# Kernel optimization log

Hardware: AMD Instinct MI355X
Metric: run time of the kernel (lower is better)

The kernel has to match this reference:

```python
import jax, jax.numpy as jnp
import numpy as np

N_NODES = 100000
N_EDGES = 1250000
D_FEAT = 64


def setup_inputs() -> dict:
    key = jax.random.key(0)
    kx, ke = jax.random.split(key)
    x = jax.random.normal(kx, (N_NODES, D_FEAT), dtype=jnp.float32)
    edge_index = jax.random.randint(ke, (2, N_EDGES), 0, N_NODES, dtype=jnp.int64)
    return {"x": x, "edge_index": edge_index}


def reference(x, edge_index):
    # propagate: scatter_nested gathers x[idxj] grouped by destination idxi
    # (a ragged per-node neighbor set); the module's sum_nested reduces each
    # group. Expressed densely and jit-ably as gather + segment-sum.
    idxi = edge_index[0, :]  # destination nodes
    idxj = edge_index[1, :]  # source nodes
    messages = x[idxj]  # [E, D] edge-level gather (memory-bound)
    out = jax.ops.segment_sum(messages, idxi, num_segments=N_NODES)  # [N, D]
    return out
```

## Files before the change

kernel.cpp:

```cpp
#include <hip/hip_runtime.h>

#define N_NODES 100000
#define N_EDGES 1250000
#define D_FEAT  64

#define NPB     256
#define NBINS   ((N_NODES + NPB - 1) / NPB)
#define BCAP    4096
#define EPB     4096
#define K1B     ((N_EDGES + EPB - 1) / EPB)
#define OVF_CAP 32768

#define CAP     48


__global__ __launch_bounds__(512) void k1_bin_kernel(
        const int* __restrict__ idxi, const int* __restrict__ idxj,
        int* __restrict__ gcursor, int* __restrict__ ovfcnt,
        int* __restrict__ ovf, int* __restrict__ binbuf) {
    __shared__ int hist[512];
    __shared__ int runstart[512];
    __shared__ int gbase[NBINS];
    __shared__ int cur[NBINS];
    __shared__ int staged[EPB];
    __shared__ unsigned short sbin[EPB];
    int t = threadIdx.x;
    hist[t] = 0;
    __syncthreads();

    long long base = (long long)blockIdx.x * EPB;
    int d[8], s[8], bn[8];
#pragma unroll
    for (int j = 0; j < 8; ++j) {
        long long e = base + t + j * 512;
        if (e < N_EDGES) {
            d[j] = idxi[e];
            s[j] = idxj[e];
            bn[j] = d[j] >> 8;
            atomicAdd(&hist[bn[j]], 1);
        } else {
            bn[j] = -1;
        }
    }
    __syncthreads();

    runstart[t] = hist[t];
    __syncthreads();
    for (int off = 1; off < 512; off <<= 1) {
        int add = (t >= off) ? runstart[t - off] : 0;
        __syncthreads();
        runstart[t] += add;
        __syncthreads();
    }
    int excl = runstart[t] - hist[t];
    __syncthreads();
    runstart[t] = excl;
    if (t < NBINS) {
        gbase[t] = hist[t] ? atomicAdd(&gcursor[t], hist[t]) : 0;
        cur[t] = 0;
    }
    __syncthreads();

#pragma unroll
    for (int j = 0; j < 8; ++j) {
        if (bn[j] >= 0) {
            int lofs = atomicAdd(&cur[bn[j]], 1);
            int idx = runstart[bn[j]] + lofs;
            staged[idx] = ((d[j] & 255) << 17) | s[j];
            sbin[idx] = (unsigned short)bn[j];
        }
    }
    __syncthreads();

    long long rem = (long long)N_EDGES - base;
    int n = (rem < EPB) ? (int)rem : EPB;
    for (int i = t; i < n; i += 512) {
        int b = sbin[i];
        int p = staged[i];
        int tgt = gbase[b] + (i - runstart[b]);
        if (tgt < BCAP) {
            binbuf[(size_t)b * BCAP + tgt] = p;
        } else {
            int op = atomicAdd(ovfcnt, 1);
            if (op < OVF_CAP) { ovf[2 * op] = b * NPB + (p >> 17); ovf[2 * op + 1] = p & 0x1FFFF; }
        }
    }
}

__global__ __launch_bounds__(1024) void k2_sort_kernel(
        const int* __restrict__ gcursor, const int* __restrict__ binbuf,
        int* __restrict__ sorted, int* __restrict__ offs, int* __restrict__ len) {
    __shared__ int cnt[NPB];
    __shared__ int excl[NPB];
    __shared__ int cur[NPB];
    __shared__ int stmp[NPB];
    int bin = blockIdx.x;
    int t = threadIdx.x;
    if (t < NPB) cnt[t] = 0;
    __syncthreads();

    int n = gcursor[bin];
    if (n > BCAP) n = BCAP;
    const int* src = binbuf + (size_t)bin * BCAP;
    int p[4];
#pragma unroll
    for (int j = 0; j < 4; ++j) {
        int i = t + j * 1024;
        p[j] = (i < n) ? src[i] : -1;
        if (p[j] >= 0) atomicAdd(&cnt[p[j] >> 17], 1);
    }
    __syncthreads();

    if (t < NPB) stmp[t] = cnt[t];
    __syncthreads();
    for (int off = 1; off < NPB; off <<= 1) {
        int v = 0;
        if (t < NPB && t >= off) v = stmp[t - off];
        __syncthreads();
        if (t < NPB) stmp[t] += v;
        __syncthreads();
    }
    if (t < NPB) {
        excl[t] = stmp[t] - cnt[t];
        cur[t] = 0;
        int node = bin * NPB + t;
        if (node < N_NODES) {
            offs[node] = bin * BCAP + excl[t];
            len[node]  = cnt[t];
        }
    }
    __syncthreads();

    int* dst = sorted + (size_t)bin * BCAP;
#pragma unroll
    for (int j = 0; j < 4; ++j) {
        if (p[j] >= 0) {
            int dl = p[j] >> 17;
            int pos = excl[dl] + atomicAdd(&cur[dl], 1);
            dst[pos] = p[j] & 0x1FFFF;
        }
    }
}

__global__ __launch_bounds__(256) void k3_gather_kernel(
        const float* __restrict__ x, const int* __restrict__ offs,
        const int* __restrict__ len, const int* __restrict__ sorted,
        float* __restrict__ out) {
    int node = blockIdx.x * 4 + (threadIdx.x >> 6);
    int lane = threadIdx.x & 63;
    if (node >= N_NODES) return;
    const int* b = sorted + offs[node];
    int l = len[node];
    int sub = lane >> 4;
    int c4  = lane & 15;

    float4 acc = make_float4(0.f, 0.f, 0.f, 0.f);
    int k = 0;
    for (; k + 8 <= l; k += 8) {
        int s0 = b[k + sub];
        int s1 = b[k + 4 + sub];
        const float4 v0 = *(const float4*)(x + (size_t)s0 * D_FEAT + c4 * 4);
        const float4 v1 = *(const float4*)(x + (size_t)s1 * D_FEAT + c4 * 4);
        acc.x += v0.x + v1.x;
        acc.y += v0.y + v1.y;
        acc.z += v0.z + v1.z;
        acc.w += v0.w + v1.w;
    }
    if (k + 4 <= l) {
        int s0 = b[k + sub];
        const float4 v0 = *(const float4*)(x + (size_t)s0 * D_FEAT + c4 * 4);
        acc.x += v0.x; acc.y += v0.y; acc.z += v0.z; acc.w += v0.w;
        k += 4;
    }
    if (k + sub < l) {
        int s0 = b[k + sub];
        const float4 v0 = *(const float4*)(x + (size_t)s0 * D_FEAT + c4 * 4);
        acc.x += v0.x; acc.y += v0.y; acc.z += v0.z; acc.w += v0.w;
    }

    acc.x += __shfl_xor(acc.x, 16, 64);
    acc.y += __shfl_xor(acc.y, 16, 64);
    acc.z += __shfl_xor(acc.z, 16, 64);
    acc.w += __shfl_xor(acc.w, 16, 64);
    acc.x += __shfl_xor(acc.x, 32, 64);
    acc.y += __shfl_xor(acc.y, 32, 64);
    acc.z += __shfl_xor(acc.z, 32, 64);
    acc.w += __shfl_xor(acc.w, 32, 64);

    if (lane < 16) {
        ((float4*)out)[(size_t)node * 16 + c4] = acc;
    }
}

__global__ __launch_bounds__(256) void ovf_fixup_kernel(
        const float* __restrict__ x, const int* __restrict__ ovfcnt,
        const int* __restrict__ ovf, float* __restrict__ out) {
    int n = *ovfcnt;
    if (n > OVF_CAP) n = OVF_CAP;
    long long total = (long long)n * 16;
    long long stride = (long long)gridDim.x * blockDim.x;
    for (long long t = blockIdx.x * blockDim.x + threadIdx.x; t < total; t += stride) {
        int e  = (int)(t >> 4);
        int fo = ((int)t & 15) << 2;
        int d = ovf[2 * e];
        int s = ovf[2 * e + 1];
        const float4 v = *(const float4*)(x + (size_t)s * D_FEAT + fo);
        float* o = out + (size_t)d * D_FEAT + fo;
        atomicAdd(o + 0, v.x);
        atomicAdd(o + 1, v.y);
        atomicAdd(o + 2, v.z);
        atomicAdd(o + 3, v.w);
    }
}


__global__ __launch_bounds__(256) void scatter_pad_kernel(
        const int* __restrict__ idxi, const int* __restrict__ idxj,
        int* __restrict__ cnt, int* __restrict__ ovfcnt,
        int* __restrict__ ovf, int* __restrict__ bucket) {
    int e = blockIdx.x * blockDim.x + threadIdx.x;
    if (e >= N_EDGES) return;
    int d = idxi[e];
    int s = idxj[e];
    int pos = atomicAdd(&cnt[d], 1);
    if (pos < CAP) {
        bucket[(size_t)d * CAP + pos] = s;
    } else {
        int op = atomicAdd(ovfcnt, 1);
        if (op < OVF_CAP) { ovf[2 * op] = d; ovf[2 * op + 1] = s; }
    }
}

__global__ __launch_bounds__(256) void gather_pad_kernel(
        const float* __restrict__ x, const int* __restrict__ cnt,
        const int* __restrict__ bucket, float* __restrict__ out) {
    int node = blockIdx.x * 4 + (threadIdx.x >> 6);
    int lane = threadIdx.x & 63;
    if (node >= N_NODES) return;
    int c = cnt[node];
    if (c > CAP) c = CAP;
    const int* b = bucket + (size_t)node * CAP;
    float acc = 0.f;
    int k = 0;
    for (; k + 4 <= c; k += 4) {
        int4 s4 = *(const int4*)(b + k);
        float a0 = x[(size_t)s4.x * D_FEAT + lane];
        float a1 = x[(size_t)s4.y * D_FEAT + lane];
        float a2 = x[(size_t)s4.z * D_FEAT + lane];
        float a3 = x[(size_t)s4.w * D_FEAT + lane];
        acc += (a0 + a1) + (a2 + a3);
    }
    for (; k < c; ++k) acc += x[(size_t)b[k] * D_FEAT + lane];
    out[(size_t)node * D_FEAT + lane] = acc;
}


__global__ __launch_bounds__(256) void zero_f4_kernel(float* __restrict__ out, int n4) {
    int i = blockIdx.x * blockDim.x + threadIdx.x;
    if (i < n4) ((float4*)out)[i] = make_float4(0.f, 0.f, 0.f, 0.f);
}

__global__ __launch_bounds__(256) void scatter_add_kernel(const float* __restrict__ x,
                                                          const int* __restrict__ idxi,
                                                          const int* __restrict__ idxj,
                                                          float* __restrict__ out) {
    int t = blockIdx.x * blockDim.x + threadIdx.x;
    int e = t >> 4;
    if (e >= N_EDGES) return;
    int fo = (t & 15) << 2;
    int dst = idxi[e];
    int src = idxj[e];
    const float4 v = *(const float4*)(x + (size_t)src * D_FEAT + fo);
    float* o = out + (size_t)dst * D_FEAT + fo;
    atomicAdd(o + 0, v.x);
    atomicAdd(o + 1, v.y);
    atomicAdd(o + 2, v.z);
    atomicAdd(o + 3, v.w);
}

extern "C" void kernel_launch(void* const* d_in, const int* in_sizes, int n_in,
                              void* d_out, int out_size, void* d_ws, size_t ws_size,
                              hipStream_t stream) {
    const float* x  = (const float*)d_in[0];
    const int*   ei = (const int*)d_in[1];
    const int*   idxi = ei;
    const int*   idxj = ei + N_EDGES;
    float* out = (float*)d_out;

    int nbe = (N_EDGES + 255) / 256;
    int gather_blocks = (N_NODES + 3) / 4;

    {
        size_t need = (512 + 16 + 2 * (size_t)OVF_CAP +
                       2 * (size_t)NBINS * BCAP + 2 * (size_t)N_NODES) * sizeof(int);
        if (ws_size >= need) {
            int* gcursor = (int*)d_ws;
            int* ovfcnt  = gcursor + 512;
            int* ovf     = ovfcnt + 16;
            int* binbuf  = ovf + 2 * OVF_CAP;
            int* sorted  = binbuf + (size_t)NBINS * BCAP;
            int* offs    = sorted + (size_t)NBINS * BCAP;
            int* len     = offs + N_NODES;

            hipMemsetAsync(gcursor, 0, (512 + 16) * sizeof(int), stream);
            k1_bin_kernel<<<K1B, 512, 0, stream>>>(idxi, idxj, gcursor, ovfcnt, ovf, binbuf);
            k2_sort_kernel<<<NBINS, 1024, 0, stream>>>(gcursor, binbuf, sorted, offs, len);
            k3_gather_kernel<<<gather_blocks, 256, 0, stream>>>(x, offs, len, sorted, out);
            ovf_fixup_kernel<<<64, 256, 0, stream>>>(x, ovfcnt, ovf, out);
            return;
        }
    }

    {
        size_t need = ((size_t)N_NODES + 16 + 2 * (size_t)OVF_CAP +
                       (size_t)N_NODES * CAP) * sizeof(int);
        if (ws_size >= need) {
            int* cnt    = (int*)d_ws;
            int* ovfcnt = cnt + N_NODES;
            int* ovf    = cnt + N_NODES + 16;
            int* bucket = ovf + 2 * OVF_CAP;

            hipMemsetAsync(cnt, 0, (N_NODES + 16) * sizeof(int), stream);
            scatter_pad_kernel<<<nbe, 256, 0, stream>>>(idxi, idxj, cnt, ovfcnt, ovf, bucket);
            gather_pad_kernel<<<gather_blocks, 256, 0, stream>>>(x, cnt, bucket, out);
            ovf_fixup_kernel<<<64, 256, 0, stream>>>(x, ovfcnt, ovf, out);
            return;
        }
    }

    int n4 = (N_NODES * D_FEAT) / 4;
    zero_f4_kernel<<<(n4 + 255) / 256, 256, 0, stream>>>(out, n4);
    long long total_threads = (long long)N_EDGES * 16;
    scatter_add_kernel<<<(int)((total_threads + 255) / 256), 256, 0, stream>>>(x, idxi, idxj, out);
}
```

Measured before the change: 147.7 us.

## Fuse per-bin sort with neighbor gather using shared-memory sorted indices

Merges the bin sort kernel and the gather kernel into one, keeping sorted source indices in shared memory instead of writing sorted/offs/len arrays to global memory. Each 1024-thread block handles one 256-node bin, with each wave summing 16 nodes sequentially. This removes a launch and the intermediate global traffic but cuts the number of independent waves for the latency-bound gather. The overflow fixup grid is also reduced.

```diff
diff --git a/kernel.cpp b/kernel.cpp
--- a/kernel.cpp
+++ b/kernel.cpp
@@ -87,13 +87,14 @@
     }
 }
 
-__global__ __launch_bounds__(1024) void k2_sort_kernel(
-        const int* __restrict__ gcursor, const int* __restrict__ binbuf,
-        int* __restrict__ sorted, int* __restrict__ offs, int* __restrict__ len) {
+__global__ __launch_bounds__(1024) void k23_fused_kernel(
+        const float* __restrict__ x, const int* __restrict__ gcursor,
+        const int* __restrict__ binbuf, float* __restrict__ out) {
     __shared__ int cnt[NPB];
     __shared__ int excl[NPB];
     __shared__ int cur[NPB];
     __shared__ int stmp[NPB];
+    __shared__ int srt[BCAP];
     int bin = blockIdx.x;
     int t = threadIdx.x;
     if (t < NPB) cnt[t] = 0;
@@ -123,72 +124,65 @@
     if (t < NPB) {
         excl[t] = stmp[t] - cnt[t];
         cur[t] = 0;
-        int node = bin * NPB + t;
-        if (node < N_NODES) {
-            offs[node] = bin * BCAP + excl[t];
-            len[node]  = cnt[t];
-        }
-    }
-    __syncthreads();
-
-    int* dst = sorted + (size_t)bin * BCAP;
+    }
+    __syncthreads();
+
 #pragma unroll
     for (int j = 0; j < 4; ++j) {
         if (p[j] >= 0) {
             int dl = p[j] >> 17;
             int pos = excl[dl] + atomicAdd(&cur[dl], 1);
-            dst[pos] = p[j] & 0x1FFFF;
-        }
-    }
-}
-
-__global__ __launch_bounds__(256) void k3_gather_kernel(
-        const float* __restrict__ x, const int* __restrict__ offs,
-        const int* __restrict__ len, const int* __restrict__ sorted,
-        float* __restrict__ out) {
-    int node = blockIdx.x * 4 + (threadIdx.x >> 6);
-    int lane = threadIdx.x & 63;
-    if (node >= N_NODES) return;
-    const int* b = sorted + offs[node];
-    int l = len[node];
-    int sub = lane >> 4;
-    int c4  = lane & 15;
-
-    float4 acc = make_float4(0.f, 0.f, 0.f, 0.f);
-    int k = 0;
-    for (; k + 8 <= l; k += 8) {
-        int s0 = b[k + sub];
-        int s1 = b[k + 4 + sub];
-        const float4 v0 = *(const float4*)(x + (size_t)s0 * D_FEAT + c4 * 4);
-        const float4 v1 = *(const float4*)(x + (size_t)s1 * D_FEAT + c4 * 4);
-        acc.x += v0.x + v1.x;
-        acc.y += v0.y + v1.y;
-        acc.z += v0.z + v1.z;
-        acc.w += v0.w + v1.w;
-    }
-    if (k + 4 <= l) {
-        int s0 = b[k + sub];
-        const float4 v0 = *(const float4*)(x + (size_t)s0 * D_FEAT + c4 * 4);
-        acc.x += v0.x; acc.y += v0.y; acc.z += v0.z; acc.w += v0.w;
-        k += 4;
-    }
-    if (k + sub < l) {
-        int s0 = b[k + sub];
-        const float4 v0 = *(const float4*)(x + (size_t)s0 * D_FEAT + c4 * 4);
-        acc.x += v0.x; acc.y += v0.y; acc.z += v0.z; acc.w += v0.w;
-    }
-
-    acc.x += __shfl_xor(acc.x, 16, 64);
-    acc.y += __shfl_xor(acc.y, 16, 64);
-    acc.z += __shfl_xor(acc.z, 16, 64);
-    acc.w += __shfl_xor(acc.w, 16, 64);
-    acc.x += __shfl_xor(acc.x, 32, 64);
-    acc.y += __shfl_xor(acc.y, 32, 64);
-    acc.z += __shfl_xor(acc.z, 32, 64);
-    acc.w += __shfl_xor(acc.w, 32, 64);
-
-    if (lane < 16) {
-        ((float4*)out)[(size_t)node * 16 + c4] = acc;
+            srt[pos] = p[j] & 0x1FFFF;
+        }
+    }
+    __syncthreads();
+
+    int wave = t >> 6;
+    int lane = t & 63;
+    int sub  = lane >> 4;
+    int c4   = lane & 15;
+    for (int i = 0; i < 16; ++i) {
+        int dloc = wave * 16 + i;
+        int node = bin * NPB + dloc;
+        if (node >= N_NODES) break;
+        int base = excl[dloc];
+        int l = cnt[dloc];
+        float4 acc = make_float4(0.f, 0.f, 0.f, 0.f);
+        int k = 0;
+        for (; k + 8 <= l; k += 8) {
+            int s0 = srt[base + k + sub];
+            int s1 = srt[base + k + 4 + sub];
+            const float4 v0 = *(const float4*)(x + (size_t)s0 * D_FEAT + c4 * 4);
+            const float4 v1 = *(const float4*)(x + (size_t)s1 * D_FEAT + c4 * 4);
+            acc.x += v0.x + v1.x;
+            acc.y += v0.y + v1.y;
+            acc.z += v0.z + v1.z;
+            acc.w += v0.w + v1.w;
+        }
+        if (k + 4 <= l) {
+            int s0 = srt[base + k + sub];
+            const float4 v0 = *(const float4*)(x + (size_t)s0 * D_FEAT + c4 * 4);
+            acc.x += v0.x; acc.y += v0.y; acc.z += v0.z; acc.w += v0.w;
+            k += 4;
+        }
+        if (k + sub < l) {
+            int s0 = srt[base + k + sub];
+            const float4 v0 = *(const float4*)(x + (size_t)s0 * D_FEAT + c4 * 4);
+            acc.x += v0.x; acc.y += v0.y; acc.z += v0.z; acc.w += v0.w;
+        }
+
+        acc.x += __shfl_xor(acc.x, 16, 64);
+        acc.y += __shfl_xor(acc.y, 16, 64);
+        acc.z += __shfl_xor(acc.z, 16, 64);
+        acc.w += __shfl_xor(acc.w, 16, 64);
+        acc.x += __shfl_xor(acc.x, 32, 64);
+        acc.y += __shfl_xor(acc.y, 32, 64);
+        acc.z += __shfl_xor(acc.z, 32, 64);
+        acc.w += __shfl_xor(acc.w, 32, 64);
+
+        if (lane < 16) {
+            ((float4*)out)[(size_t)node * 16 + c4] = acc;
+        }
     }
 }
 
@@ -292,21 +286,17 @@
 
     {
         size_t need = (512 + 16 + 2 * (size_t)OVF_CAP +
-                       2 * (size_t)NBINS * BCAP + 2 * (size_t)N_NODES) * sizeof(int);
+                       (size_t)NBINS * BCAP) * sizeof(int);
         if (ws_size >= need) {
             int* gcursor = (int*)d_ws;
             int* ovfcnt  = gcursor + 512;
             int* ovf     = ovfcnt + 16;
             int* binbuf  = ovf + 2 * OVF_CAP;
-            int* sorted  = binbuf + (size_t)NBINS * BCAP;
-            int* offs    = sorted + (size_t)NBINS * BCAP;
-            int* len     = offs + N_NODES;
 
             hipMemsetAsync(gcursor, 0, (512 + 16) * sizeof(int), stream);
             k1_bin_kernel<<<K1B, 512, 0, stream>>>(idxi, idxj, gcursor, ovfcnt, ovf, binbuf);
-            k2_sort_kernel<<<NBINS, 1024, 0, stream>>>(gcursor, binbuf, sorted, offs, len);
-            k3_gather_kernel<<<gather_blocks, 256, 0, stream>>>(x, offs, len, sorted, out);
-            ovf_fixup_kernel<<<64, 256, 0, stream>>>(x, ovfcnt, ovf, out);
+            k23_fused_kernel<<<NBINS, 1024, 0, stream>>>(x, gcursor, binbuf, out);
+            ovf_fixup_kernel<<<16, 256, 0, stream>>>(x, ovfcnt, ovf, out);
             return;
         }
     }
@@ -323,7 +313,7 @@
             hipMemsetAsync(cnt, 0, (N_NODES + 16) * sizeof(int), stream);
             scatter_pad_kernel<<<nbe, 256, 0, stream>>>(idxi, idxj, cnt, ovfcnt, ovf, bucket);
             gather_pad_kernel<<<gather_blocks, 256, 0, stream>>>(x, cnt, bucket, out);
-            ovf_fixup_kernel<<<64, 256, 0, stream>>>(x, ovfcnt, ovf, out);
+            ovf_fixup_kernel<<<16, 256, 0, stream>>>(x, ovfcnt, ovf, out);
             return;
         }
     }
```

Measured after the change: 140.8 us. -4.7%, faster.
